# Kernel optimization log

Measured on AMD Instinct MI355X. Metric: run time of the kernel, lower is better.

## Reference

```python
import jax, jax.numpy as jnp
import numpy as np

EPS = 1e-5          # layer_norm_eps
N_HEADS = 32
N_KV_HEADS = 8
N_REP = N_HEADS // N_KV_HEADS   # GQA repeat factor = 4
HEAD_DIM = 64
ROPE_THETA = 10000.0


def layer_norm(x, w, b):
    # standard LayerNorm: (x - mean) / sqrt(var + eps) * w + b  (biased var)
    mean = jnp.mean(x, axis=-1, keepdims=True)
    var = jnp.mean((x - mean) ** 2, axis=-1, keepdims=True)
    return (x - mean) / jnp.sqrt(var + EPS) * w + b


def apply_rope(x):
    # x: [B, S, H, D]; interleaved-pair rotary embedding (llama2.c style)
    B, S, H, D = x.shape
    freqs = 1.0 / (ROPE_THETA ** (jnp.arange(0, D, 2, dtype=jnp.float32) / D))  # [D/2]
    ang = jnp.arange(S, dtype=jnp.float32)[:, None] * freqs[None, :]            # [S, D/2]
    cos = jnp.cos(ang)[None, :, None, :]
    sin = jnp.sin(ang)[None, :, None, :]
    xr = x[..., 0::2]
    xi = x[..., 1::2]
    out_r = xr * cos - xi * sin
    out_i = xr * sin + xi * cos
    return jnp.stack([out_r, out_i], axis=-1).reshape(B, S, H, D)


def setup_inputs() -> dict:
    key = jax.random.key(0)
    ks = jax.random.split(key, 9)
    B, S, D, HID = 1, 2048, 2048, 5632
    KV = N_KV_HEADS * HEAD_DIM  # 512
    s = 0.02
    return {
        "x": jax.random.normal(ks[0], (B, S, D), dtype=jnp.float32),
        "attention_mask": jnp.ones((B, S), dtype=jnp.int32),
        "wq": jax.random.normal(ks[1], (D, D), dtype=jnp.float32) * s,
        "wk": jax.random.normal(ks[2], (D, KV), dtype=jnp.float32) * s,
        "wv": jax.random.normal(ks[3], (D, KV), dtype=jnp.float32) * s,
        "wo": jax.random.normal(ks[4], (D, D), dtype=jnp.float32) * s,
        "w1": jax.random.normal(ks[5], (D, HID), dtype=jnp.float32) * s,
        "w2": jax.random.normal(ks[6], (HID, D), dtype=jnp.float32) * s,
        "w3": jax.random.normal(ks[7], (D, HID), dtype=jnp.float32) * s,
        "ln1_w": jnp.ones((D,), dtype=jnp.float32),
        "ln1_b": jnp.zeros((D,), dtype=jnp.float32),
        "ln2_w": jnp.ones((D,), dtype=jnp.float32),
        "ln2_b": jnp.zeros((D,), dtype=jnp.float32),
    }


def reference(x, attention_mask, wq, wk, wv, wo, w1, w2, w3,
              ln1_w, ln1_b, ln2_w, ln2_b):
    B, S, D = x.shape
    # 1) pre-attention LayerNorm
    h = layer_norm(x, ln1_w, ln1_b)
    # 2) GQA attention with RoPE
    q = (h @ wq).reshape(B, S, N_HEADS, HEAD_DIM)
    k = (h @ wk).reshape(B, S, N_KV_HEADS, HEAD_DIM)
    v = (h @ wv).reshape(B, S, N_KV_HEADS, HEAD_DIM)
    q = apply_rope(q)
    k = apply_rope(k)
    # repeat_interleave KV heads to match query heads
    k = jnp.repeat(k, N_REP, axis=2)
    v = jnp.repeat(v, N_REP, axis=2)
    q = q.transpose(0, 2, 1, 3)  # [B,H,S,D]
    k = k.transpose(0, 2, 1, 3)
    v = v.transpose(0, 2, 1, 3)
    scores = jnp.einsum("bhqd,bhkd->bhqk", q, k) / jnp.sqrt(
        jnp.asarray(HEAD_DIM, dtype=q.dtype))
    mask = attention_mask[:, None, None, :]  # [B,1,1,S] applied on key axis
    scores = jnp.where(mask == 0, -jnp.inf, scores)
    attn = jax.nn.softmax(scores, axis=-1)
    out = jnp.einsum("bhqk,bhkd->bhqd", attn, v)
    out = out.transpose(0, 2, 1, 3).reshape(B, S, N_HEADS * HEAD_DIM)
    attn_out = out @ wo
    # 3) residual
    x1 = x + attn_out
    # 4) post-attention LayerNorm + SwiGLU FFN
    h2 = layer_norm(x1, ln2_w, ln2_b)
    ffn = (jax.nn.silu(h2 @ w1) * (h2 @ w3)) @ w2
    # 5) residual
    return x1 + ffn
```

## Files before the change

### kernel.cpp

```cpp
#include <hip/hip_runtime.h>

#define S_LEN 2048
#define D_MODEL 2048
#define HID_DIM 5632
#define KV_DIM 512
#define QKV_DIM 3072
#define NH 32
#define NKV 8
#define HD 64
#define PS_LD 132

typedef __bf16 bf16x8 __attribute__((ext_vector_type(8)));
typedef float f32x4 __attribute__((ext_vector_type(4)));

__device__ __forceinline__ float bf2f(ushort u) {
    union { unsigned i; float f; } x; x.i = ((unsigned)u) << 16; return x.f;
}
__device__ __forceinline__ ushort f2bf(float f) {
    union { float f; unsigned i; } x; x.f = f;
    unsigned r = x.i + 0x7FFFu + ((x.i >> 16) & 1u);
    return (ushort)(r >> 16);
}
__device__ __forceinline__ void gll16(const ushort* g, ushort* l) {
    __builtin_amdgcn_global_load_lds(
        (const __attribute__((address_space(1))) void*)g,
        (__attribute__((address_space(3))) void*)l, 16, 0, 0);
}
__device__ __forceinline__ int swz_rd(int g, int qlane) { return ((g ^ (qlane & 7)) * 8); }

template<int BN>
__global__ __launch_bounds__(256) void gemm_bt(
    const ushort* __restrict__ A, const ushort* __restrict__ Bt, ushort* __restrict__ C,
    int K, int lda, int ldb, int ldc, float alpha)
{
    constexpr int TN = BN / 32;
    __shared__ ushort As[128 * 64];
    __shared__ ushort Bs[BN * 64];

    const int tid  = threadIdx.x;
    const int wave = tid >> 6;
    const int lane = tid & 63;
    const int qlane = lane & 15;
    const int quad  = lane >> 4;
    const int wm = (wave >> 1) * 64;
    const int wn = (wave & 1) * (BN / 2);
    const long bm0 = (long)blockIdx.y * 128;
    const long bn0 = (long)blockIdx.x * BN;

    f32x4 acc[4][TN];
#pragma unroll
    for (int i = 0; i < 4; i++)
#pragma unroll
        for (int j = 0; j < TN; j++) acc[i][j] = (f32x4){0.f,0.f,0.f,0.f};

    const int rsub = tid >> 3;
    const int csw  = ((tid & 7) ^ (rsub & 7)) * 8;

    for (int k0 = 0; k0 < K; k0 += 64) {
#pragma unroll
        for (int i = 0; i < 4; i++)
            gll16(A + (bm0 + i*32 + rsub) * (long)lda + k0 + csw, As + (i*256 + wave*64)*8);
#pragma unroll
        for (int i = 0; i < BN/32; i++)
            gll16(Bt + (bn0 + i*32 + rsub) * (long)ldb + k0 + csw, Bs + (i*256 + wave*64)*8);
        __syncthreads();
#pragma unroll
        for (int kk = 0; kk < 64; kk += 32) {
            bf16x8 af[4], bfr[TN];
#pragma unroll
            for (int t = 0; t < 4; t++)
                af[t] = *(const bf16x8*)(As + (wm + t*16 + qlane)*64 + swz_rd((kk>>3) + quad, qlane));
#pragma unroll
            for (int t = 0; t < TN; t++)
                bfr[t] = *(const bf16x8*)(Bs + (wn + t*16 + qlane)*64 + swz_rd((kk>>3) + quad, qlane));
#pragma unroll
            for (int tm = 0; tm < 4; tm++)
#pragma unroll
                for (int tn = 0; tn < TN; tn++)
                    acc[tm][tn] = __builtin_amdgcn_mfma_f32_16x16x32_bf16(
                        af[tm], bfr[tn], acc[tm][tn], 0, 0, 0);
        }
        __syncthreads();
    }

#pragma unroll
    for (int tm = 0; tm < 4; tm++) {
        const long row = bm0 + wm + tm*16 + quad*4;
#pragma unroll
        for (int tn = 0; tn < TN; tn++) {
            const long col = bn0 + wn + tn*16 + qlane;
#pragma unroll
            for (int i = 0; i < 4; i++)
                C[(row + i) * ldc + col] = f2bf(acc[tm][tn][i] * alpha);
        }
    }
}

__global__ __launch_bounds__(256) void gemm_bt_res(
    const ushort* __restrict__ A, const ushort* __restrict__ Bt,
    const float* __restrict__ Res, float* __restrict__ Out,
    int K, int lda, int ldb, int ldc)
{
    __shared__ ushort As[128 * 64];
    __shared__ ushort Bs[64 * 64];

    const int tid  = threadIdx.x;
    const int wave = tid >> 6;
    const int lane = tid & 63;
    const int qlane = lane & 15;
    const int quad  = lane >> 4;
    const int wm = (wave >> 1) * 64;
    const int wn = (wave & 1) * 32;
    const long bm0 = (long)blockIdx.y * 128;
    const long bn0 = (long)blockIdx.x * 64;

    f32x4 acc[4][2];
#pragma unroll
    for (int i = 0; i < 4; i++)
#pragma unroll
        for (int j = 0; j < 2; j++) acc[i][j] = (f32x4){0.f,0.f,0.f,0.f};

    const int rsub = tid >> 3;
    const int csw  = ((tid & 7) ^ (rsub & 7)) * 8;

    for (int k0 = 0; k0 < K; k0 += 64) {
#pragma unroll
        for (int i = 0; i < 4; i++)
            gll16(A + (bm0 + i*32 + rsub) * (long)lda + k0 + csw, As + (i*256 + wave*64)*8);
#pragma unroll
        for (int i = 0; i < 2; i++)
            gll16(Bt + (bn0 + i*32 + rsub) * (long)ldb + k0 + csw, Bs + (i*256 + wave*64)*8);
        __syncthreads();
#pragma unroll
        for (int kk = 0; kk < 64; kk += 32) {
            bf16x8 af[4], bfr[2];
#pragma unroll
            for (int t = 0; t < 4; t++)
                af[t] = *(const bf16x8*)(As + (wm + t*16 + qlane)*64 + swz_rd((kk>>3) + quad, qlane));
#pragma unroll
            for (int t = 0; t < 2; t++)
                bfr[t] = *(const bf16x8*)(Bs + (wn + t*16 + qlane)*64 + swz_rd((kk>>3) + quad, qlane));
#pragma unroll
            for (int tm = 0; tm < 4; tm++)
#pragma unroll
                for (int tn = 0; tn < 2; tn++)
                    acc[tm][tn] = __builtin_amdgcn_mfma_f32_16x16x32_bf16(
                        af[tm], bfr[tn], acc[tm][tn], 0, 0, 0);
        }
        __syncthreads();
    }

#pragma unroll
    for (int tm = 0; tm < 4; tm++) {
        const long row = bm0 + wm + tm*16 + quad*4;
#pragma unroll
        for (int tn = 0; tn < 2; tn++) {
            const long col = bn0 + wn + tn*16 + qlane;
#pragma unroll
            for (int i = 0; i < 4; i++)
                Out[(row + i) * ldc + col] = Res[(row + i) * ldc + col] + acc[tm][tn][i];
        }
    }
}

__global__ __launch_bounds__(256) void gemm_ffn13(
    const ushort* __restrict__ A, const ushort* __restrict__ B1t,
    const ushort* __restrict__ B3t, ushort* __restrict__ G)
{
    __shared__ ushort As[128 * 64];
    __shared__ ushort B1s[64 * 64];
    __shared__ ushort B3s[64 * 64];

    const int tid  = threadIdx.x;
    const int wave = tid >> 6;
    const int lane = tid & 63;
    const int qlane = lane & 15;
    const int quad  = lane >> 4;
    const int wm = (wave >> 1) * 64;
    const int wn = (wave & 1) * 32;
    const long bm0 = (long)blockIdx.y * 128;
    const long bn0 = (long)blockIdx.x * 64;

    f32x4 a1[4][2], a3[4][2];
#pragma unroll
    for (int i = 0; i < 4; i++)
#pragma unroll
        for (int j = 0; j < 2; j++) { a1[i][j] = (f32x4){0.f,0.f,0.f,0.f}; a3[i][j] = a1[i][j]; }

    const int rsub = tid >> 3;
    const int csw  = ((tid & 7) ^ (rsub & 7)) * 8;

    for (int k0 = 0; k0 < D_MODEL; k0 += 64) {
#pragma unroll
        for (int i = 0; i < 4; i++)
            gll16(A + (bm0 + i*32 + rsub) * (long)D_MODEL + k0 + csw, As + (i*256 + wave*64)*8);
#pragma unroll
        for (int i = 0; i < 2; i++) {
            gll16(B1t + (bn0 + i*32 + rsub) * (long)D_MODEL + k0 + csw, B1s + (i*256 + wave*64)*8);
            gll16(B3t + (bn0 + i*32 + rsub) * (long)D_MODEL + k0 + csw, B3s + (i*256 + wave*64)*8);
        }
        __syncthreads();
#pragma unroll
        for (int kk = 0; kk < 64; kk += 32) {
            bf16x8 af[4], b1f[2], b3f[2];
#pragma unroll
            for (int t = 0; t < 4; t++)
                af[t] = *(const bf16x8*)(As + (wm + t*16 + qlane)*64 + swz_rd((kk>>3) + quad, qlane));
#pragma unroll
            for (int t = 0; t < 2; t++) {
                b1f[t] = *(const bf16x8*)(B1s + (wn + t*16 + qlane)*64 + swz_rd((kk>>3) + quad, qlane));
                b3f[t] = *(const bf16x8*)(B3s + (wn + t*16 + qlane)*64 + swz_rd((kk>>3) + quad, qlane));
            }
#pragma unroll
            for (int tm = 0; tm < 4; tm++)
#pragma unroll
                for (int tn = 0; tn < 2; tn++) {
                    a1[tm][tn] = __builtin_amdgcn_mfma_f32_16x16x32_bf16(af[tm], b1f[tn], a1[tm][tn], 0,0,0);
                    a3[tm][tn] = __builtin_amdgcn_mfma_f32_16x16x32_bf16(af[tm], b3f[tn], a3[tm][tn], 0,0,0);
                }
        }
        __syncthreads();
    }

#pragma unroll
    for (int tm = 0; tm < 4; tm++) {
        const long row = bm0 + wm + tm*16 + quad*4;
#pragma unroll
        for (int tn = 0; tn < 2; tn++) {
            const long col = bn0 + wn + tn*16 + qlane;
#pragma unroll
            for (int i = 0; i < 4; i++) {
                const float u = a1[tm][tn][i];
                const float g = u / (1.f + __expf(-u)) * a3[tm][tn][i];
                G[(row + i) * HID_DIM + col] = f2bf(g);
            }
        }
    }
}

__global__ __launch_bounds__(256) void flash_attn_k(
    const ushort* __restrict__ qkv, const ushort* __restrict__ vT,
    ushort* __restrict__ attn)
{
    __shared__ ushort Ks[128 * HD];
    __shared__ ushort Vs[HD * 128];
    __shared__ ushort Ps[128 * PS_LD];

    const int h = blockIdx.x;
    const int kvh = h >> 2;
    const int q0 = blockIdx.y * 128;

    const int tid = threadIdx.x;
    const int wave = tid >> 6;
    const int lane = tid & 63;
    const int qlane = lane & 15;
    const int quad = lane >> 4;
    const int wm = wave * 32;

    bf16x8 qf[2][2];
#pragma unroll
    for (int mt = 0; mt < 2; mt++)
#pragma unroll
        for (int ks = 0; ks < 2; ks++)
            qf[mt][ks] = *(const bf16x8*)(qkv + (long)(q0 + wm + mt*16 + qlane) * QKV_DIM
                                          + h * HD + ks*32 + quad*8);

    f32x4 o[2][4];
#pragma unroll
    for (int i = 0; i < 2; i++)
#pragma unroll
        for (int j = 0; j < 4; j++) o[i][j] = (f32x4){0.f,0.f,0.f,0.f};
    float mrow[2][4], lrow[2][4];
#pragma unroll
    for (int i = 0; i < 2; i++)
#pragma unroll
        for (int j = 0; j < 4; j++) { mrow[i][j] = -1e30f; lrow[i][j] = 0.f; }

    const int rsub = tid >> 3;
    const int cswk = ((tid & 7) ^ (rsub & 7)) * 8;
    const int rsv  = tid >> 4;
    const int cswv = ((tid & 15) ^ (rsv & 7)) * 8;
    const ushort* kbase = qkv + D_MODEL + kvh * HD;
    const ushort* vbase = vT + (long)kvh * HD * S_LEN;

    for (int k0 = 0; k0 < S_LEN; k0 += 128) {
        __syncthreads();
#pragma unroll
        for (int i = 0; i < 4; i++)
            gll16(kbase + (long)(k0 + i*32 + rsub) * QKV_DIM + cswk, Ks + (i*256 + wave*64)*8);
#pragma unroll
        for (int i = 0; i < 4; i++)
            gll16(vbase + (long)(i*16 + rsv) * S_LEN + k0 + cswv, Vs + (i*256 + wave*64)*8);
        __syncthreads();

        f32x4 s[2][8];
#pragma unroll
        for (int mt = 0; mt < 2; mt++)
#pragma unroll
            for (int nt = 0; nt < 8; nt++) s[mt][nt] = (f32x4){0.f,0.f,0.f,0.f};
#pragma unroll
        for (int ks = 0; ks < 2; ks++) {
            bf16x8 kf[8];
#pragma unroll
            for (int nt = 0; nt < 8; nt++)
                kf[nt] = *(const bf16x8*)(Ks + (nt*16 + qlane)*64 + swz_rd(ks*4 + quad, qlane));
#pragma unroll
            for (int mt = 0; mt < 2; mt++)
#pragma unroll
                for (int nt = 0; nt < 8; nt++)
                    s[mt][nt] = __builtin_amdgcn_mfma_f32_16x16x32_bf16(
                        qf[mt][ks], kf[nt], s[mt][nt], 0, 0, 0);
        }

#pragma unroll
        for (int mt = 0; mt < 2; mt++) {
            float mn[4], rs[4];
#pragma unroll
            for (int i = 0; i < 4; i++) {
                float v = s[mt][0][i];
#pragma unroll
                for (int nt = 1; nt < 8; nt++) v = fmaxf(v, s[mt][nt][i]);
                mn[i] = v;
            }
#pragma unroll
            for (int i = 0; i < 4; i++) {
#pragma unroll
                for (int msk = 1; msk < 16; msk <<= 1)
                    mn[i] = fmaxf(mn[i], __shfl_xor(mn[i], msk, 64));
                mn[i] = fmaxf(mn[i], mrow[mt][i]);
            }
#pragma unroll
            for (int i = 0; i < 4; i++) {
                rs[i] = 0.f;
#pragma unroll
                for (int nt = 0; nt < 8; nt++) {
                    const float pv = __expf(s[mt][nt][i] - mn[i]);
                    s[mt][nt][i] = pv;
                    rs[i] += pv;
                }
#pragma unroll
                for (int msk = 1; msk < 16; msk <<= 1)
                    rs[i] += __shfl_xor(rs[i], msk, 64);
                const float alpha = __expf(mrow[mt][i] - mn[i]);
                mrow[mt][i] = mn[i];
                lrow[mt][i] = lrow[mt][i] * alpha + rs[i];
#pragma unroll
                for (int dt = 0; dt < 4; dt++) o[mt][dt][i] *= alpha;
            }
#pragma unroll
            for (int nt = 0; nt < 8; nt++)
#pragma unroll
                for (int i = 0; i < 4; i++)
                    Ps[(wm + mt*16 + quad*4 + i)*PS_LD + nt*16 + qlane] = f2bf(s[mt][nt][i]);
        }
        __syncthreads();

#pragma unroll
        for (int kt = 0; kt < 4; kt++) {
            bf16x8 pf[2], vf[4];
#pragma unroll
            for (int mt = 0; mt < 2; mt++)
                pf[mt] = *(const bf16x8*)(Ps + (wm + mt*16 + qlane)*PS_LD + kt*32 + quad*8);
#pragma unroll
            for (int dt = 0; dt < 4; dt++)
                vf[dt] = *(const bf16x8*)(Vs + (dt*16 + qlane)*128 + swz_rd(kt*4 + quad, qlane));
#pragma unroll
            for (int mt = 0; mt < 2; mt++)
#pragma unroll
                for (int dt = 0; dt < 4; dt++)
                    o[mt][dt] = __builtin_amdgcn_mfma_f32_16x16x32_bf16(
                        pf[mt], vf[dt], o[mt][dt], 0, 0, 0);
        }
    }

#pragma unroll
    for (int mt = 0; mt < 2; mt++)
#pragma unroll
        for (int i = 0; i < 4; i++) {
            const float inv = 1.f / lrow[mt][i];
            const long row = q0 + wm + mt*16 + quad*4 + i;
#pragma unroll
            for (int dt = 0; dt < 4; dt++)
                attn[row * D_MODEL + h*HD + dt*16 + qlane] = f2bf(o[mt][dt][i] * inv);
        }
}

__global__ __launch_bounds__(256) void layernorm_k(
    const float* __restrict__ x, const float* __restrict__ w,
    const float* __restrict__ b, ushort* __restrict__ out)
{
    __shared__ float red[4];
    const int row = blockIdx.x;
    const float* xr = x + (long)row * D_MODEL;
    const int wv_ = threadIdx.x >> 6, ln = threadIdx.x & 63;

    float v[8];
    float s = 0.f;
#pragma unroll
    for (int i = 0; i < 8; i++) { v[i] = xr[threadIdx.x + i*256]; s += v[i]; }
#pragma unroll
    for (int o = 32; o; o >>= 1) s += __shfl_xor(s, o, 64);
    if (ln == 0) red[wv_] = s;
    __syncthreads();
    const float mean = (red[0]+red[1]+red[2]+red[3]) * (1.f / D_MODEL);
    __syncthreads();

    float var = 0.f;
#pragma unroll
    for (int i = 0; i < 8; i++) { const float d = v[i] - mean; var += d*d; }
#pragma unroll
    for (int o = 32; o; o >>= 1) var += __shfl_xor(var, o, 64);
    if (ln == 0) red[wv_] = var;
    __syncthreads();
    var = (red[0]+red[1]+red[2]+red[3]) * (1.f / D_MODEL);
    const float rstd = rsqrtf(var + 1e-5f);

#pragma unroll
    for (int i = 0; i < 8; i++) {
        const int c = threadIdx.x + i*256;
        out[(long)row * D_MODEL + c] = f2bf((v[i] - mean) * rstd * w[c] + b[c]);
    }
}

__global__ __launch_bounds__(256) void rope_k(ushort* __restrict__ x, int H, int ld, float scale)
{
    const int idx = blockIdx.x * 256 + threadIdx.x;
    const int fi = idx & 31;
    const int h_ = (idx >> 5) % H;
    const int s  = (idx >> 5) / H;
    const float freq = powf(10000.f, -(float)(2*fi) / 64.f);
    float sn, cs;
    sincosf((float)s * freq, &sn, &cs);
    ushort* p = x + (long)s * ld + h_ * HD + fi * 2;
    const float xr = bf2f(p[0]), xi = bf2f(p[1]);
    p[0] = f2bf((xr * cs - xi * sn) * scale);
    p[1] = f2bf((xr * sn + xi * cs) * scale);
}

__global__ void transcvt_k(const float* __restrict__ in, ushort* __restrict__ out,
                           int R, int C, int ldin, int ldout)
{
    __shared__ float tile[32][33];
    const int c0 = blockIdx.x * 32, r0 = blockIdx.y * 32;
    for (int i = threadIdx.y; i < 32; i += 8) {
        const int r = r0 + i, c = c0 + threadIdx.x;
        if (r < R && c < C) tile[i][threadIdx.x] = in[(long)r * ldin + c];
    }
    __syncthreads();
    for (int i = threadIdx.y; i < 32; i += 8) {
        const int c = c0 + i, r = r0 + threadIdx.x;
        if (r < R && c < C) out[(long)c * ldout + r] = f2bf(tile[threadIdx.x][i]);
    }
}

__global__ void transpose_k(const ushort* __restrict__ in, ushort* __restrict__ out,
                            int R, int C, int ldin, int ldout, long inB, long outB)
{
    __shared__ ushort tile[32][33];
    const long b = blockIdx.z;
    in += b * inB; out += b * outB;
    const int c0 = blockIdx.x * 32, r0 = blockIdx.y * 32;
    for (int i = threadIdx.y; i < 32; i += 8) {
        const int r = r0 + i, c = c0 + threadIdx.x;
        if (r < R && c < C) tile[i][threadIdx.x] = in[(long)r * ldin + c];
    }
    __syncthreads();
    for (int i = threadIdx.y; i < 32; i += 8) {
        const int c = c0 + i, r = r0 + threadIdx.x;
        if (r < R && c < C) out[(long)c * ldout + r] = tile[threadIdx.x][i];
    }
}

extern "C" void kernel_launch(void* const* d_in, const int* in_sizes, int n_in,
                              void* d_out, int out_size, void* d_ws, size_t ws_size,
                              hipStream_t stream)
{
    const float* x   = (const float*)d_in[0];
    const float* wq  = (const float*)d_in[2];
    const float* wk  = (const float*)d_in[3];
    const float* wv  = (const float*)d_in[4];
    const float* wo  = (const float*)d_in[5];
    const float* w1  = (const float*)d_in[6];
    const float* w2  = (const float*)d_in[7];
    const float* w3  = (const float*)d_in[8];
    const float* ln1w = (const float*)d_in[9];
    const float* ln1b = (const float*)d_in[10];
    const float* ln2w = (const float*)d_in[11];
    const float* ln2b = (const float*)d_in[12];
    float* out = (float*)d_out;

    char* p = (char*)d_ws;
    auto alloc = [&](size_t bytes) {
        char* r = p; p += (bytes + 255) & ~(size_t)255; return r;
    };
    ushort* h      = (ushort*)alloc((size_t)S_LEN * D_MODEL * 2);
    ushort* qkv    = (ushort*)alloc((size_t)S_LEN * QKV_DIM * 2);
    ushort* vT     = (ushort*)alloc((size_t)NKV * HD * S_LEN * 2);
    ushort* attn   = (ushort*)alloc((size_t)S_LEN * D_MODEL * 2);
    float*  x1     = (float*) alloc((size_t)S_LEN * D_MODEL * 4);
    ushort* g1     = (ushort*)alloc((size_t)S_LEN * HID_DIM * 2);
    ushort* wqkvT  = (ushort*)alloc((size_t)QKV_DIM * D_MODEL * 2);
    ushort* woT    = (ushort*)alloc((size_t)D_MODEL * D_MODEL * 2);
    ushort* w1T    = (ushort*)alloc((size_t)D_MODEL * HID_DIM * 2);
    ushort* w2T    = (ushort*)alloc((size_t)D_MODEL * HID_DIM * 2);
    ushort* w3T    = (ushort*)alloc((size_t)D_MODEL * HID_DIM * 2);

    ushort* h2 = h;

    const dim3 blk(256);
    const dim3 tb(32, 8);

    transcvt_k<<<dim3(64, 64),  tb, 0, stream>>>(wq, wqkvT, D_MODEL, D_MODEL, D_MODEL, D_MODEL);
    transcvt_k<<<dim3(16, 64),  tb, 0, stream>>>(wk, wqkvT + (size_t)D_MODEL*D_MODEL, D_MODEL, KV_DIM, KV_DIM, D_MODEL);
    transcvt_k<<<dim3(16, 64),  tb, 0, stream>>>(wv, wqkvT + (size_t)(D_MODEL+KV_DIM)*D_MODEL, D_MODEL, KV_DIM, KV_DIM, D_MODEL);
    transcvt_k<<<dim3(64, 64),  tb, 0, stream>>>(wo, woT, D_MODEL, D_MODEL, D_MODEL, D_MODEL);
    transcvt_k<<<dim3(176, 64), tb, 0, stream>>>(w1, w1T, D_MODEL, HID_DIM, HID_DIM, D_MODEL);
    transcvt_k<<<dim3(176, 64), tb, 0, stream>>>(w3, w3T, D_MODEL, HID_DIM, HID_DIM, D_MODEL);
    transcvt_k<<<dim3(64, 176), tb, 0, stream>>>(w2, w2T, HID_DIM, D_MODEL, D_MODEL, HID_DIM);

    layernorm_k<<<S_LEN, blk, 0, stream>>>(x, ln1w, ln1b, h);

    gemm_bt<64><<<dim3(QKV_DIM/64, 16), blk, 0, stream>>>(
        h, wqkvT, qkv, D_MODEL, D_MODEL, D_MODEL, QKV_DIM, 1.f);

    rope_k<<<(S_LEN*NH*32)/256, blk, 0, stream>>>(qkv, NH, QKV_DIM, 1.f);
    rope_k<<<(S_LEN*NKV*32)/256, blk, 0, stream>>>(qkv + D_MODEL, NKV, QKV_DIM, 0.125f);

    transpose_k<<<dim3(2, 64, NKV), tb, 0, stream>>>(
        qkv + D_MODEL + KV_DIM, vT, S_LEN, HD, QKV_DIM, S_LEN, (long)HD, (long)HD * S_LEN);

    flash_attn_k<<<dim3(NH, S_LEN/128), blk, 0, stream>>>(qkv, vT, attn);

    gemm_bt_res<<<dim3(32, 16), blk, 0, stream>>>(
        attn, woT, x, x1, D_MODEL, D_MODEL, D_MODEL, D_MODEL);

    layernorm_k<<<S_LEN, blk, 0, stream>>>(x1, ln2w, ln2b, h2);
    gemm_ffn13<<<dim3(HID_DIM/64, 16), blk, 0, stream>>>(h2, w1T, w3T, g1);
    gemm_bt_res<<<dim3(32, 16), blk, 0, stream>>>(
        g1, w2T, x1, out, HID_DIM, HID_DIM, HID_DIM, D_MODEL);
}
```

Before: 634.4 us.

## Widen GEMM tiles to 128, vectorize transpose-convert and RoPE, add MFMA priority

```diff
diff --git a/kernel.cpp b/kernel.cpp
--- a/kernel.cpp
+++ b/kernel.cpp
@@ -12,6 +12,8 @@
 
 typedef __bf16 bf16x8 __attribute__((ext_vector_type(8)));
 typedef float f32x4 __attribute__((ext_vector_type(4)));
+typedef ushort us4 __attribute__((ext_vector_type(4)));
+typedef ushort us8 __attribute__((ext_vector_type(8)));
 
 __device__ __forceinline__ float bf2f(ushort u) {
     union { unsigned i; float f; } x; x.i = ((unsigned)u) << 16; return x.f;
@@ -96,13 +98,15 @@
     }
 }
 
+template<int BN>
 __global__ __launch_bounds__(256) void gemm_bt_res(
     const ushort* __restrict__ A, const ushort* __restrict__ Bt,
     const float* __restrict__ Res, float* __restrict__ Out,
     int K, int lda, int ldb, int ldc)
 {
+    constexpr int TN = BN / 32;
     __shared__ ushort As[128 * 64];
-    __shared__ ushort Bs[64 * 64];
+    __shared__ ushort Bs[BN * 64];
 
     const int tid  = threadIdx.x;
     const int wave = tid >> 6;
@@ -110,15 +114,15 @@
     const int qlane = lane & 15;
     const int quad  = lane >> 4;
     const int wm = (wave >> 1) * 64;
-    const int wn = (wave & 1) * 32;
+    const int wn = (wave & 1) * (BN / 2);
     const long bm0 = (long)blockIdx.y * 128;
-    const long bn0 = (long)blockIdx.x * 64;
-
-    f32x4 acc[4][2];
+    const long bn0 = (long)blockIdx.x * BN;
+
+    f32x4 acc[4][TN];
 #pragma unroll
     for (int i = 0; i < 4; i++)
 #pragma unroll
-        for (int j = 0; j < 2; j++) acc[i][j] = (f32x4){0.f,0.f,0.f,0.f};
+        for (int j = 0; j < TN; j++) acc[i][j] = (f32x4){0.f,0.f,0.f,0.f};
 
     const int rsub = tid >> 3;
     const int csw  = ((tid & 7) ^ (rsub & 7)) * 8;
@@ -128,22 +132,22 @@
         for (int i = 0; i < 4; i++)
             gll16(A + (bm0 + i*32 + rsub) * (long)lda + k0 + csw, As + (i*256 + wave*64)*8);
 #pragma unroll
-        for (int i = 0; i < 2; i++)
+        for (int i = 0; i < BN/32; i++)
             gll16(Bt + (bn0 + i*32 + rsub) * (long)ldb + k0 + csw, Bs + (i*256 + wave*64)*8);
         __syncthreads();
 #pragma unroll
         for (int kk = 0; kk < 64; kk += 32) {
-            bf16x8 af[4], bfr[2];
+            bf16x8 af[4], bfr[TN];
 #pragma unroll
             for (int t = 0; t < 4; t++)
                 af[t] = *(const bf16x8*)(As + (wm + t*16 + qlane)*64 + swz_rd((kk>>3) + quad, qlane));
 #pragma unroll
-            for (int t = 0; t < 2; t++)
+            for (int t = 0; t < TN; t++)
                 bfr[t] = *(const bf16x8*)(Bs + (wn + t*16 + qlane)*64 + swz_rd((kk>>3) + quad, qlane));
 #pragma unroll
             for (int tm = 0; tm < 4; tm++)
 #pragma unroll
-                for (int tn = 0; tn < 2; tn++)
+                for (int tn = 0; tn < TN; tn++)
                     acc[tm][tn] = __builtin_amdgcn_mfma_f32_16x16x32_bf16(
                         af[tm], bfr[tn], acc[tm][tn], 0, 0, 0);
         }
@@ -154,7 +158,7 @@
     for (int tm = 0; tm < 4; tm++) {
         const long row = bm0 + wm + tm*16 + quad*4;
 #pragma unroll
-        for (int tn = 0; tn < 2; tn++) {
+        for (int tn = 0; tn < TN; tn++) {
             const long col = bn0 + wn + tn*16 + qlane;
 #pragma unroll
             for (int i = 0; i < 4; i++)
@@ -168,8 +172,8 @@
     const ushort* __restrict__ B3t, ushort* __restrict__ G)
 {
     __shared__ ushort As[128 * 64];
-    __shared__ ushort B1s[64 * 64];
-    __shared__ ushort B3s[64 * 64];
+    __shared__ ushort B1s[128 * 64];
+    __shared__ ushort B3s[128 * 64];
 
     const int tid  = threadIdx.x;
     const int wave = tid >> 6;
@@ -177,15 +181,15 @@
     const int qlane = lane & 15;
     const int quad  = lane >> 4;
     const int wm = (wave >> 1) * 64;
-    const int wn = (wave & 1) * 32;
+    const int wn = (wave & 1) * 64;
     const long bm0 = (long)blockIdx.y * 128;
-    const long bn0 = (long)blockIdx.x * 64;
-
-    f32x4 a1[4][2], a3[4][2];
+    const long bn0 = (long)blockIdx.x * 128;
+
+    f32x4 a1[4][4], a3[4][4];
 #pragma unroll
     for (int i = 0; i < 4; i++)
 #pragma unroll
-        for (int j = 0; j < 2; j++) { a1[i][j] = (f32x4){0.f,0.f,0.f,0.f}; a3[i][j] = a1[i][j]; }
+        for (int j = 0; j < 4; j++) { a1[i][j] = (f32x4){0.f,0.f,0.f,0.f}; a3[i][j] = a1[i][j]; }
 
     const int rsub = tid >> 3;
     const int csw  = ((tid & 7) ^ (rsub & 7)) * 8;
@@ -195,26 +199,26 @@
         for (int i = 0; i < 4; i++)
             gll16(A + (bm0 + i*32 + rsub) * (long)D_MODEL + k0 + csw, As + (i*256 + wave*64)*8);
 #pragma unroll
-        for (int i = 0; i < 2; i++) {
+        for (int i = 0; i < 4; i++) {
             gll16(B1t + (bn0 + i*32 + rsub) * (long)D_MODEL + k0 + csw, B1s + (i*256 + wave*64)*8);
             gll16(B3t + (bn0 + i*32 + rsub) * (long)D_MODEL + k0 + csw, B3s + (i*256 + wave*64)*8);
         }
         __syncthreads();
 #pragma unroll
         for (int kk = 0; kk < 64; kk += 32) {
-            bf16x8 af[4], b1f[2], b3f[2];
+            bf16x8 af[4], b1f[4], b3f[4];
 #pragma unroll
             for (int t = 0; t < 4; t++)
                 af[t] = *(const bf16x8*)(As + (wm + t*16 + qlane)*64 + swz_rd((kk>>3) + quad, qlane));
 #pragma unroll
-            for (int t = 0; t < 2; t++) {
+            for (int t = 0; t < 4; t++) {
                 b1f[t] = *(const bf16x8*)(B1s + (wn + t*16 + qlane)*64 + swz_rd((kk>>3) + quad, qlane));
                 b3f[t] = *(const bf16x8*)(B3s + (wn + t*16 + qlane)*64 + swz_rd((kk>>3) + quad, qlane));
             }
 #pragma unroll
             for (int tm = 0; tm < 4; tm++)
 #pragma unroll
-                for (int tn = 0; tn < 2; tn++) {
+                for (int tn = 0; tn < 4; tn++) {
                     a1[tm][tn] = __builtin_amdgcn_mfma_f32_16x16x32_bf16(af[tm], b1f[tn], a1[tm][tn], 0,0,0);
                     a3[tm][tn] = __builtin_amdgcn_mfma_f32_16x16x32_bf16(af[tm], b3f[tn], a3[tm][tn], 0,0,0);
                 }
@@ -226,7 +230,7 @@
     for (int tm = 0; tm < 4; tm++) {
         const long row = bm0 + wm + tm*16 + quad*4;
 #pragma unroll
-        for (int tn = 0; tn < 2; tn++) {
+        for (int tn = 0; tn < 4; tn++) {
             const long col = bn0 + wn + tn*16 + qlane;
 #pragma unroll
             for (int i = 0; i < 4; i++) {
@@ -304,12 +308,14 @@
 #pragma unroll
             for (int nt = 0; nt < 8; nt++)
                 kf[nt] = *(const bf16x8*)(Ks + (nt*16 + qlane)*64 + swz_rd(ks*4 + quad, qlane));
+            __builtin_amdgcn_s_setprio(1);
 #pragma unroll
             for (int mt = 0; mt < 2; mt++)
 #pragma unroll
                 for (int nt = 0; nt < 8; nt++)
                     s[mt][nt] = __builtin_amdgcn_mfma_f32_16x16x32_bf16(
                         qf[mt][ks], kf[nt], s[mt][nt], 0, 0, 0);
+            __builtin_amdgcn_s_setprio(0);
         }
 
 #pragma unroll
@@ -364,12 +370,14 @@
 #pragma unroll
             for (int dt = 0; dt < 4; dt++)
                 vf[dt] = *(const bf16x8*)(Vs + (dt*16 + qlane)*128 + swz_rd(kt*4 + quad, qlane));
+            __builtin_amdgcn_s_setprio(1);
 #pragma unroll
             for (int mt = 0; mt < 2; mt++)
 #pragma unroll
                 for (int dt = 0; dt < 4; dt++)
                     o[mt][dt] = __builtin_amdgcn_mfma_f32_16x16x32_bf16(
                         pf[mt], vf[dt], o[mt][dt], 0, 0, 0);
+            __builtin_amdgcn_s_setprio(0);
         }
     }
 
@@ -425,31 +433,48 @@
 __global__ __launch_bounds__(256) void rope_k(ushort* __restrict__ x, int H, int ld, float scale)
 {
     const int idx = blockIdx.x * 256 + threadIdx.x;
-    const int fi = idx & 31;
-    const int h_ = (idx >> 5) % H;
-    const int s  = (idx >> 5) / H;
-    const float freq = powf(10000.f, -(float)(2*fi) / 64.f);
-    float sn, cs;
-    sincosf((float)s * freq, &sn, &cs);
-    ushort* p = x + (long)s * ld + h_ * HD + fi * 2;
-    const float xr = bf2f(p[0]), xi = bf2f(p[1]);
-    p[0] = f2bf((xr * cs - xi * sn) * scale);
-    p[1] = f2bf((xr * sn + xi * cs) * scale);
-}
-
-__global__ void transcvt_k(const float* __restrict__ in, ushort* __restrict__ out,
-                           int R, int C, int ldin, int ldout)
-{
-    __shared__ float tile[32][33];
-    const int c0 = blockIdx.x * 32, r0 = blockIdx.y * 32;
-    for (int i = threadIdx.y; i < 32; i += 8) {
-        const int r = r0 + i, c = c0 + threadIdx.x;
-        if (r < R && c < C) tile[i][threadIdx.x] = in[(long)r * ldin + c];
+    const int g  = idx & 7;
+    const int h_ = (idx >> 3) % H;
+    const int s  = (idx >> 3) / H;
+    ushort* p = x + (long)s * ld + h_ * HD + g * 8;
+    us8 v = *(const us8*)p;
+#pragma unroll
+    for (int j = 0; j < 4; j++) {
+        const int fi = g * 4 + j;
+        const float freq = exp2f((float)fi * -0.41524101186f);
+        float sn, cs;
+        sincosf((float)s * freq, &sn, &cs);
+        const float xr = bf2f(v[2*j]), xi = bf2f(v[2*j+1]);
+        v[2*j]   = f2bf((xr * cs - xi * sn) * scale);
+        v[2*j+1] = f2bf((xr * sn + xi * cs) * scale);
+    }
+    *(us8*)p = v;
+}
+
+__global__ __launch_bounds__(256) void transcvt_k(
+    const float* __restrict__ in, ushort* __restrict__ out, int ldin, int ldout)
+{
+    __shared__ ushort tile[64][68];
+    const long c0 = (long)blockIdx.x * 64, r0 = (long)blockIdx.y * 64;
+    const int tid = threadIdx.x;
+
+    const int lr = tid >> 4, lc = (tid & 15) * 4;
+#pragma unroll
+    for (int i = 0; i < 4; i++) {
+        const float4 f = *(const float4*)(in + (r0 + lr + i*16) * (long)ldin + c0 + lc);
+        us4 u; u[0] = f2bf(f.x); u[1] = f2bf(f.y); u[2] = f2bf(f.z); u[3] = f2bf(f.w);
+        *(us4*)&tile[lr + i*16][lc] = u;
     }
     __syncthreads();
-    for (int i = threadIdx.y; i < 32; i += 8) {
-        const int c = c0 + i, r = r0 + threadIdx.x;
-        if (r < R && c < C) out[(long)c * ldout + r] = f2bf(tile[threadIdx.x][i]);
+
+    const int oc = tid >> 3, orc = (tid & 7) * 8;
+#pragma unroll
+    for (int i = 0; i < 2; i++) {
+        const int c = oc + i*32;
+        us8 o;
+#pragma unroll
+        for (int j = 0; j < 8; j++) o[j] = tile[orc + j][c];
+        *(us8*)(out + (c0 + c) * (long)ldout + r0 + orc) = o;
     }
 }
 
@@ -510,32 +535,32 @@
     const dim3 blk(256);
     const dim3 tb(32, 8);
 
-    transcvt_k<<<dim3(64, 64),  tb, 0, stream>>>(wq, wqkvT, D_MODEL, D_MODEL, D_MODEL, D_MODEL);
-    transcvt_k<<<dim3(16, 64),  tb, 0, stream>>>(wk, wqkvT + (size_t)D_MODEL*D_MODEL, D_MODEL, KV_DIM, KV_DIM, D_MODEL);
-    transcvt_k<<<dim3(16, 64),  tb, 0, stream>>>(wv, wqkvT + (size_t)(D_MODEL+KV_DIM)*D_MODEL, D_MODEL, KV_DIM, KV_DIM, D_MODEL);
-    transcvt_k<<<dim3(64, 64),  tb, 0, stream>>>(wo, woT, D_MODEL, D_MODEL, D_MODEL, D_MODEL);
-    transcvt_k<<<dim3(176, 64), tb, 0, stream>>>(w1, w1T, D_MODEL, HID_DIM, HID_DIM, D_MODEL);
-    transcvt_k<<<dim3(176, 64), tb, 0, stream>>>(w3, w3T, D_MODEL, HID_DIM, HID_DIM, D_MODEL);
-    transcvt_k<<<dim3(64, 176), tb, 0, stream>>>(w2, w2T, HID_DIM, D_MODEL, D_MODEL, HID_DIM);
+    transcvt_k<<<dim3(32, 32), blk, 0, stream>>>(wq, wqkvT, D_MODEL, D_MODEL);
+    transcvt_k<<<dim3(8,  32), blk, 0, stream>>>(wk, wqkvT + (size_t)D_MODEL*D_MODEL, KV_DIM, D_MODEL);
+    transcvt_k<<<dim3(8,  32), blk, 0, stream>>>(wv, wqkvT + (size_t)(D_MODEL+KV_DIM)*D_MODEL, KV_DIM, D_MODEL);
+    transcvt_k<<<dim3(32, 32), blk, 0, stream>>>(wo, woT, D_MODEL, D_MODEL);
+    transcvt_k<<<dim3(88, 32), blk, 0, stream>>>(w1, w1T, HID_DIM, D_MODEL);
+    transcvt_k<<<dim3(88, 32), blk, 0, stream>>>(w3, w3T, HID_DIM, D_MODEL);
+    transcvt_k<<<dim3(32, 88), blk, 0, stream>>>(w2, w2T, D_MODEL, HID_DIM);
 
     layernorm_k<<<S_LEN, blk, 0, stream>>>(x, ln1w, ln1b, h);
 
-    gemm_bt<64><<<dim3(QKV_DIM/64, 16), blk, 0, stream>>>(
+    gemm_bt<128><<<dim3(QKV_DIM/128, 16), blk, 0, stream>>>(
         h, wqkvT, qkv, D_MODEL, D_MODEL, D_MODEL, QKV_DIM, 1.f);
 
-    rope_k<<<(S_LEN*NH*32)/256, blk, 0, stream>>>(qkv, NH, QKV_DIM, 1.f);
-    rope_k<<<(S_LEN*NKV*32)/256, blk, 0, stream>>>(qkv + D_MODEL, NKV, QKV_DIM, 0.125f);
+    rope_k<<<(S_LEN*NH*8)/256, blk, 0, stream>>>(qkv, NH, QKV_DIM, 1.f);
+    rope_k<<<(S_LEN*NKV*8)/256, blk, 0, stream>>>(qkv + D_MODEL, NKV, QKV_DIM, 0.125f);
 
     transpose_k<<<dim3(2, 64, NKV), tb, 0, stream>>>(
         qkv + D_MODEL + KV_DIM, vT, S_LEN, HD, QKV_DIM, S_LEN, (long)HD, (long)HD * S_LEN);
 
     flash_attn_k<<<dim3(NH, S_LEN/128), blk, 0, stream>>>(qkv, vT, attn);
 
-    gemm_bt_res<<<dim3(32, 16), blk, 0, stream>>>(
+    gemm_bt_res<128><<<dim3(16, 16), blk, 0, stream>>>(
         attn, woT, x, x1, D_MODEL, D_MODEL, D_MODEL, D_MODEL);
 
     layernorm_k<<<S_LEN, blk, 0, stream>>>(x1, ln2w, ln2b, h2);
-    gemm_ffn13<<<dim3(HID_DIM/64, 16), blk, 0, stream>>>(h2, w1T, w3T, g1);
-    gemm_bt_res<<<dim3(32, 16), blk, 0, stream>>>(
+    gemm_ffn13<<<dim3(HID_DIM/128, 16), blk, 0, stream>>>(h2, w1T, w3T, g1);
+    gemm_bt_res<128><<<dim3(16, 16), blk, 0, stream>>>(
         g1, w2T, x1, out, HID_DIM, HID_DIM, HID_DIM, D_MODEL);
 }
```

Result: slower. 693.9 us (+9.4%).

## Vectorize layernorm/rope, merge weight transposes into one kernel, add MFMA setprio

Applied to the files above, without the earlier changes.

```diff
diff --git a/kernel.cpp b/kernel.cpp
--- a/kernel.cpp
+++ b/kernel.cpp
@@ -12,6 +12,8 @@
 
 typedef __bf16 bf16x8 __attribute__((ext_vector_type(8)));
 typedef float f32x4 __attribute__((ext_vector_type(4)));
+typedef ushort us4 __attribute__((ext_vector_type(4)));
+typedef ushort us8 __attribute__((ext_vector_type(8)));
 
 __device__ __forceinline__ float bf2f(ushort u) {
     union { unsigned i; float f; } x; x.i = ((unsigned)u) << 16; return x.f;
@@ -304,12 +306,14 @@
 #pragma unroll
             for (int nt = 0; nt < 8; nt++)
                 kf[nt] = *(const bf16x8*)(Ks + (nt*16 + qlane)*64 + swz_rd(ks*4 + quad, qlane));
+            __builtin_amdgcn_s_setprio(1);
 #pragma unroll
             for (int mt = 0; mt < 2; mt++)
 #pragma unroll
                 for (int nt = 0; nt < 8; nt++)
                     s[mt][nt] = __builtin_amdgcn_mfma_f32_16x16x32_bf16(
                         qf[mt][ks], kf[nt], s[mt][nt], 0, 0, 0);
+            __builtin_amdgcn_s_setprio(0);
         }
 
 #pragma unroll
@@ -364,12 +368,14 @@
 #pragma unroll
             for (int dt = 0; dt < 4; dt++)
                 vf[dt] = *(const bf16x8*)(Vs + (dt*16 + qlane)*128 + swz_rd(kt*4 + quad, qlane));
+            __builtin_amdgcn_s_setprio(1);
 #pragma unroll
             for (int mt = 0; mt < 2; mt++)
 #pragma unroll
                 for (int dt = 0; dt < 4; dt++)
                     o[mt][dt] = __builtin_amdgcn_mfma_f32_16x16x32_bf16(
                         pf[mt], vf[dt], o[mt][dt], 0, 0, 0);
+            __builtin_amdgcn_s_setprio(0);
         }
     }
 
@@ -391,13 +397,13 @@
 {
     __shared__ float red[4];
     const int row = blockIdx.x;
-    const float* xr = x + (long)row * D_MODEL;
-    const int wv_ = threadIdx.x >> 6, ln = threadIdx.x & 63;
-
-    float v[8];
-    float s = 0.f;
-#pragma unroll
-    for (int i = 0; i < 8; i++) { v[i] = xr[threadIdx.x + i*256]; s += v[i]; }
+    const int tid = threadIdx.x;
+    const float* xr = x + (long)row * D_MODEL + tid * 8;
+    const int wv_ = tid >> 6, ln = tid & 63;
+
+    float4 v0 = *(const float4*)xr;
+    float4 v1 = *(const float4*)(xr + 4);
+    float s = v0.x + v0.y + v0.z + v0.w + v1.x + v1.y + v1.z + v1.w;
 #pragma unroll
     for (int o = 32; o; o >>= 1) s += __shfl_xor(s, o, 64);
     if (ln == 0) red[wv_] = s;
@@ -405,9 +411,10 @@
     const float mean = (red[0]+red[1]+red[2]+red[3]) * (1.f / D_MODEL);
     __syncthreads();
 
+    float e[8] = {v0.x, v0.y, v0.z, v0.w, v1.x, v1.y, v1.z, v1.w};
     float var = 0.f;
 #pragma unroll
-    for (int i = 0; i < 8; i++) { const float d = v[i] - mean; var += d*d; }
+    for (int i = 0; i < 8; i++) { const float d = e[i] - mean; var += d*d; }
 #pragma unroll
     for (int o = 32; o; o >>= 1) var += __shfl_xor(var, o, 64);
     if (ln == 0) red[wv_] = var;
@@ -415,41 +422,82 @@
     var = (red[0]+red[1]+red[2]+red[3]) * (1.f / D_MODEL);
     const float rstd = rsqrtf(var + 1e-5f);
 
-#pragma unroll
-    for (int i = 0; i < 8; i++) {
-        const int c = threadIdx.x + i*256;
-        out[(long)row * D_MODEL + c] = f2bf((v[i] - mean) * rstd * w[c] + b[c]);
-    }
-}
-
-__global__ __launch_bounds__(256) void rope_k(ushort* __restrict__ x, int H, int ld, float scale)
+    const float4 w0 = *(const float4*)(w + tid*8), w1 = *(const float4*)(w + tid*8 + 4);
+    const float4 b0 = *(const float4*)(b + tid*8), b1 = *(const float4*)(b + tid*8 + 4);
+    const float wv8[8] = {w0.x,w0.y,w0.z,w0.w,w1.x,w1.y,w1.z,w1.w};
+    const float bv8[8] = {b0.x,b0.y,b0.z,b0.w,b1.x,b1.y,b1.z,b1.w};
+    us8 o8;
+#pragma unroll
+    for (int i = 0; i < 8; i++)
+        o8[i] = f2bf((e[i] - mean) * rstd * wv8[i] + bv8[i]);
+    *(us8*)(out + (long)row * D_MODEL + tid*8) = o8;
+}
+
+#define ROPE_H 40
+__global__ __launch_bounds__(256) void rope_k(ushort* __restrict__ x)
 {
     const int idx = blockIdx.x * 256 + threadIdx.x;
-    const int fi = idx & 31;
-    const int h_ = (idx >> 5) % H;
-    const int s  = (idx >> 5) / H;
-    const float freq = powf(10000.f, -(float)(2*fi) / 64.f);
-    float sn, cs;
-    sincosf((float)s * freq, &sn, &cs);
-    ushort* p = x + (long)s * ld + h_ * HD + fi * 2;
-    const float xr = bf2f(p[0]), xi = bf2f(p[1]);
-    p[0] = f2bf((xr * cs - xi * sn) * scale);
-    p[1] = f2bf((xr * sn + xi * cs) * scale);
-}
-
-__global__ void transcvt_k(const float* __restrict__ in, ushort* __restrict__ out,
-                           int R, int C, int ldin, int ldout)
-{
-    __shared__ float tile[32][33];
-    const int c0 = blockIdx.x * 32, r0 = blockIdx.y * 32;
-    for (int i = threadIdx.y; i < 32; i += 8) {
-        const int r = r0 + i, c = c0 + threadIdx.x;
-        if (r < R && c < C) tile[i][threadIdx.x] = in[(long)r * ldin + c];
+    const int g  = idx & 7;
+    const int h_ = (idx >> 3) % ROPE_H;
+    const int s  = (idx >> 3) / ROPE_H;
+    const float scale = (h_ < NH) ? 1.f : 0.125f;
+    ushort* p = x + (long)s * QKV_DIM + h_ * HD + g * 8;
+    us8 v = *(const us8*)p;
+#pragma unroll
+    for (int j = 0; j < 4; j++) {
+        const int fi = g * 4 + j;
+        const float freq = exp2f((float)fi * -0.41524101186f);
+        float sn, cs;
+        sincosf((float)s * freq, &sn, &cs);
+        const float xr = bf2f(v[2*j]), xi = bf2f(v[2*j+1]);
+        v[2*j]   = f2bf((xr * cs - xi * sn) * scale);
+        v[2*j+1] = f2bf((xr * sn + xi * cs) * scale);
+    }
+    *(us8*)p = v;
+}
+
+struct TcvtDesc {
+    const float* src[7];
+    ushort* dst[7];
+    int ldin[7];
+    int ldout[7];
+    int gx[7];
+    int blk0[8];
+};
+__global__ __launch_bounds__(256) void transcvt_all_k(TcvtDesc d)
+{
+    const int bid = blockIdx.x;
+    int seg = 0;
+#pragma unroll
+    for (int i = 1; i < 7; i++) if (bid >= d.blk0[i]) seg = i;
+    const int lb = bid - d.blk0[seg];
+    const int gx = d.gx[seg];
+    const int bx = lb % gx, by = lb / gx;
+    const float* in = d.src[seg];
+    ushort* out = d.dst[seg];
+    const int ldin = d.ldin[seg], ldout = d.ldout[seg];
+
+    __shared__ ushort tile[64][68];
+    const long c0 = (long)bx * 64, r0 = (long)by * 64;
+    const int tid = threadIdx.x;
+
+    const int lr = tid >> 4, lc = (tid & 15) * 4;
+#pragma unroll
+    for (int i = 0; i < 4; i++) {
+        const float4 f = *(const float4*)(in + (r0 + lr + i*16) * (long)ldin + c0 + lc);
+        us4 u; u[0] = f2bf(f.x); u[1] = f2bf(f.y); u[2] = f2bf(f.z); u[3] = f2bf(f.w);
+        *(us4*)&tile[lr + i*16][lc] = u;
     }
     __syncthreads();
-    for (int i = threadIdx.y; i < 32; i += 8) {
-        const int c = c0 + i, r = r0 + threadIdx.x;
-        if (r < R && c < C) out[(long)c * ldout + r] = f2bf(tile[threadIdx.x][i]);
+
+    const int oc = tid >> 3, orc = (tid & 7) * 8;
+#pragma unroll
+    for (int i = 0; i < 2; i++) {
+        const int c = oc + i*32;
+        us8 o;
+#pragma unroll
+        for (int j = 0; j < 8; j++) o[j] = tile[orc + j][c];
+        *(us8*)(out + (c0 + c) * (long)ldout + r0 + orc) = o;
     }
 }
 
@@ -510,21 +558,27 @@
     const dim3 blk(256);
     const dim3 tb(32, 8);
 
-    transcvt_k<<<dim3(64, 64),  tb, 0, stream>>>(wq, wqkvT, D_MODEL, D_MODEL, D_MODEL, D_MODEL);
-    transcvt_k<<<dim3(16, 64),  tb, 0, stream>>>(wk, wqkvT + (size_t)D_MODEL*D_MODEL, D_MODEL, KV_DIM, KV_DIM, D_MODEL);
-    transcvt_k<<<dim3(16, 64),  tb, 0, stream>>>(wv, wqkvT + (size_t)(D_MODEL+KV_DIM)*D_MODEL, D_MODEL, KV_DIM, KV_DIM, D_MODEL);
-    transcvt_k<<<dim3(64, 64),  tb, 0, stream>>>(wo, woT, D_MODEL, D_MODEL, D_MODEL, D_MODEL);
-    transcvt_k<<<dim3(176, 64), tb, 0, stream>>>(w1, w1T, D_MODEL, HID_DIM, HID_DIM, D_MODEL);
-    transcvt_k<<<dim3(176, 64), tb, 0, stream>>>(w3, w3T, D_MODEL, HID_DIM, HID_DIM, D_MODEL);
-    transcvt_k<<<dim3(64, 176), tb, 0, stream>>>(w2, w2T, HID_DIM, D_MODEL, D_MODEL, HID_DIM);
+    TcvtDesc d;
+    d.src[0]=wq; d.src[1]=wk; d.src[2]=wv; d.src[3]=wo; d.src[4]=w1; d.src[5]=w3; d.src[6]=w2;
+    d.dst[0]=wqkvT;
+    d.dst[1]=wqkvT + (size_t)D_MODEL*D_MODEL;
+    d.dst[2]=wqkvT + (size_t)(D_MODEL+KV_DIM)*D_MODEL;
+    d.dst[3]=woT; d.dst[4]=w1T; d.dst[5]=w3T; d.dst[6]=w2T;
+    d.ldin[0]=D_MODEL; d.ldin[1]=KV_DIM;  d.ldin[2]=KV_DIM;  d.ldin[3]=D_MODEL;
+    d.ldin[4]=HID_DIM; d.ldin[5]=HID_DIM; d.ldin[6]=D_MODEL;
+    d.ldout[0]=D_MODEL; d.ldout[1]=D_MODEL; d.ldout[2]=D_MODEL; d.ldout[3]=D_MODEL;
+    d.ldout[4]=D_MODEL; d.ldout[5]=D_MODEL; d.ldout[6]=HID_DIM;
+    d.gx[0]=32; d.gx[1]=8; d.gx[2]=8; d.gx[3]=32; d.gx[4]=88; d.gx[5]=88; d.gx[6]=32;
+    d.blk0[0]=0; d.blk0[1]=1024; d.blk0[2]=1280; d.blk0[3]=1536; d.blk0[4]=2560;
+    d.blk0[5]=5376; d.blk0[6]=8192; d.blk0[7]=11008;
+    transcvt_all_k<<<11008, blk, 0, stream>>>(d);
 
     layernorm_k<<<S_LEN, blk, 0, stream>>>(x, ln1w, ln1b, h);
 
     gemm_bt<64><<<dim3(QKV_DIM/64, 16), blk, 0, stream>>>(
         h, wqkvT, qkv, D_MODEL, D_MODEL, D_MODEL, QKV_DIM, 1.f);
 
-    rope_k<<<(S_LEN*NH*32)/256, blk, 0, stream>>>(qkv, NH, QKV_DIM, 1.f);
-    rope_k<<<(S_LEN*NKV*32)/256, blk, 0, stream>>>(qkv + D_MODEL, NKV, QKV_DIM, 0.125f);
+    rope_k<<<(S_LEN*ROPE_H*8)/256, blk, 0, stream>>>(qkv);
 
     transpose_k<<<dim3(2, 64, NKV), tb, 0, stream>>>(
         qkv + D_MODEL + KV_DIM, vT, S_LEN, HD, QKV_DIM, S_LEN, (long)HD, (long)HD * S_LEN);
```

Result: faster. 566.0 us (-10.8%).
